# Kernel tuning notes

Hardware: AMD Instinct MI355X
Metric: run time of the kernel (lower is better)

Reference implementation:

```python
import jax, jax.numpy as jnp
import numpy as np

G = 16                 # grid side -> 4096 voxels
N_GRID = G ** 3
N_NODES = 4096         # protein nodes
DEG = 256              # node neighbors per grid voxel
HID = 64               # MPNN hidden == ResNet in_channels
NUM_CLASSES = 20
BN = np.float32(1.0 / np.sqrt(1.0 + 1e-5))  # eval-mode BatchNorm3d (mean=0, var=1, gamma=1, beta=0)


def _lin(key, fi, fo):
    return jax.random.normal(key, (fi, fo), jnp.float32) * (fi ** -0.5)


def _cw(key, o, i, k):
    return jax.random.normal(key, (o, i, k, k, k), jnp.float32) * ((i * k ** 3) ** -0.5)


def setup_inputs() -> dict:
    key = jax.random.key(0)
    ks = jax.random.split(key, 32)
    n_edges = N_GRID * DEG
    # every grid voxel receives exactly DEG messages (bincount never zero)
    edge_i = jax.random.randint(ks[0], (n_edges,), 0, N_NODES, dtype=jnp.int32)
    edge_j = jnp.repeat(jnp.arange(N_GRID, dtype=jnp.int32), DEG)
    edge_index = jnp.stack([edge_i, edge_j])  # [2, E]

    node_embedding = jax.random.normal(ks[1], (N_NODES, HID), jnp.float32)
    node_pos = jax.random.uniform(ks[2], (N_NODES, 3), jnp.float32)
    gx = (jnp.arange(G, dtype=jnp.float32) + 0.5) / G
    gd, gh, gw = jnp.meshgrid(gx, gx, gx, indexing='ij')
    grid_pos = jnp.stack([gd, gh, gw], -1).reshape(N_GRID, 3)

    z = lambda n: jnp.zeros((n,), jnp.float32)
    return {
        'node_embedding': node_embedding, 'node_pos': node_pos,
        'grid_pos': grid_pos, 'edge_index': edge_index,
        # MPNN edge / message / update MLPs
        'ew1': _lin(ks[3], 6, HID), 'eb1': z(HID), 'ew2': _lin(ks[4], HID, HID), 'eb2': z(HID),
        'mw1': _lin(ks[5], 2 * HID, HID), 'mb1': z(HID), 'mw2': _lin(ks[6], HID, HID), 'mb2': z(HID),
        'uw1': _lin(ks[7], HID, HID), 'ub1': z(HID), 'uw2': _lin(ks[8], HID, HID), 'ub2': z(HID),
        # ResNet3D: 3 Blocks (conv3 a, conv3 b, conv5 shortcut) with channels 64->64, 64->128, 128->256
        'c1a': _cw(ks[9], 64, 64, 3), 'c1b': _cw(ks[10], 64, 64, 3), 'c1s': _cw(ks[11], 64, 64, 5),
        'c2a': _cw(ks[12], 128, 64, 3), 'c2b': _cw(ks[13], 128, 128, 3), 'c2s': _cw(ks[14], 128, 64, 5),
        'c3a': _cw(ks[15], 256, 128, 3), 'c3b': _cw(ks[16], 256, 256, 3), 'c3s': _cw(ks[17], 256, 128, 5),
        'fcw': _lin(ks[18], 256, NUM_CLASSES), 'fcb': z(NUM_CLASSES),
    }


def _mlp(x, w1, b1, w2, b2):
    return jax.nn.silu(x @ w1 + b1) @ w2 + b2


def _conv(x, w, p):
    return jax.lax.conv_general_dilated(
        x, w, window_strides=(1, 1, 1), padding=[(p, p)] * 3,
        dimension_numbers=('NCDHW', 'OIDHW', 'NCDHW'))


def _block(x, wa, wb, ws):
    out = jax.nn.relu(_conv(x, wa, 1) * BN)
    out = _conv(out, wb, 1) * BN
    sc = _conv(x, ws, 2) * BN
    return jax.nn.relu(out + sc)


def reference(node_embedding, node_pos, grid_pos, edge_index,
              ew1, eb1, ew2, eb2, mw1, mb1, mw2, mb2, uw1, ub1, uw2, ub2,
              c1a, c1b, c1s, c2a, c2b, c2s, c3a, c3b, c3s, fcw, fcb):
    i, j = edge_index[0], edge_index[1]
    # ---- MPNN: gather, edge MLP, message MLP, scatter-mean, update MLP ----
    edge_attr = jnp.concatenate([node_pos[i], grid_pos[j]], axis=-1)        # [E, 6]
    pos_emb = _mlp(edge_attr, ew1, eb1, ew2, eb2)                           # [E, H]
    msg = _mlp(jnp.concatenate([node_embedding[i], pos_emb], -1),
               mw1, mb1, mw2, mb2)                                          # [E, H]
    agg = jax.ops.segment_sum(msg, j, num_segments=N_GRID)                  # [N_GRID, H]
    cnt = jax.ops.segment_sum(jnp.ones((msg.shape[0],), msg.dtype), j,
                              num_segments=N_GRID)
    grid_feat = _mlp(agg / cnt[:, None], uw1, ub1, uw2, ub2)                # [N_GRID, H]
    # ---- ResNet3D over the grid volume ----
    x = grid_feat.T.reshape(1, HID, G, G, G) * BN                           # instance_norm1 (eval BN)
    x = _block(x, c1a, c1b, c1s)
    x = _block(x, c2a, c2b, c2s)
    x = _block(x, c3a, c3b, c3s)
    pooled = jnp.max(x, axis=(2, 3, 4))                                     # max_pool3d(kernel=spatial)
    return pooled @ fcw + fcb                                               # [1, NUM_CLASSES]
```

## Files before the change

kernel.cpp:

```cpp
#include <hip/hip_runtime.h>
#include <math.h>

#define BN_S 0.9999950000374997f

typedef _Float16 half8 __attribute__((ext_vector_type(8)));
typedef float f32x4 __attribute__((ext_vector_type(4)));

__device__ __forceinline__ float silu_f(float x) {
    return __fdividef(x, 1.0f + __expf(-x));
}

__device__ __forceinline__ void gld16(const void* g, void* l) {
    __builtin_amdgcn_global_load_lds(
        (const __attribute__((address_space(1))) void*)g,
        (__attribute__((address_space(3))) void*)l, 16, 0, 0);
}

__global__ __launch_bounds__(64) void prep_w_k(
    const float* __restrict__ ew2, const float* __restrict__ mw1,
    const float* __restrict__ mw2, const float* __restrict__ uw1,
    const float* __restrict__ mb2, const float* __restrict__ ub1,
    float* __restrict__ W_mu, float* __restrict__ b_mu,
    _Float16* __restrict__ wemt_h, _Float16* __restrict__ wemt_l)
{
    const int k = blockIdx.x, c = threadIdx.x;
    float s = 0.f;
    for (int m = 0; m < 64; m++) s = fmaf(ew2[k*64 + m], mw1[(64 + m)*64 + c], s);
    {
        const int q = k >> 5, kg = (k >> 3) & 3, jj = k & 7;
        const int sl = q*256 + c*4 + kg;
        const int p = sl ^ ((sl >> 3) & 7);
        const _Float16 h = (_Float16)s;
        const _Float16 l = (_Float16)(s - (float)h);
        wemt_h[p*8 + jj] = h;
        wemt_l[p*8 + jj] = l;
    }
    float s2 = 0.f;
    for (int m = 0; m < 64; m++) s2 = fmaf(mw2[k*64 + m], uw1[m*64 + c], s2);
    W_mu[k*64 + c] = s2;
    if (k == 0) {
        float s3 = ub1[c];
        for (int m = 0; m < 64; m++) s3 = fmaf(mb2[m], uw1[m*64 + c], s3);
        b_mu[c] = s3;
    }
}

__global__ __launch_bounds__(64) void prep_nodes_k(
    const float* __restrict__ node_embedding, const float* __restrict__ node_pos,
    const float* __restrict__ grid_pos, const float* __restrict__ ew1,
    const float* __restrict__ eb1, const float* __restrict__ mw1,
    const float* __restrict__ mb1, const float* __restrict__ eb2,
    float* __restrict__ a_node, float* __restrict__ g_vox, float* __restrict__ n_node)
{
    const int v = blockIdx.x, c = threadIdx.x;
    const float p0 = node_pos[v*3], p1 = node_pos[v*3 + 1], p2 = node_pos[v*3 + 2];
    a_node[v*64 + c] = fmaf(p0, ew1[c], fmaf(p1, ew1[64 + c], fmaf(p2, ew1[128 + c], eb1[c])));
    const float q0 = grid_pos[v*3], q1 = grid_pos[v*3 + 1], q2 = grid_pos[v*3 + 2];
    g_vox[v*64 + c] = fmaf(q0, ew1[192 + c], fmaf(q1, ew1[256 + c], q2 * ew1[320 + c]));
    float s = mb1[c];
    for (int k = 0; k < 64; k++) s = fmaf(node_embedding[v*64 + k], mw1[k*64 + c], s);
    for (int k = 0; k < 64; k++) s = fmaf(eb2[k], mw1[(64 + k)*64 + c], s);
    n_node[v*64 + c] = s;
}

template<int K3, int NCOG, int NCH>
__global__ __launch_bounds__(256) void wsplit_k(
    const float* __restrict__ w, _Float16* __restrict__ dh, _Float16* __restrict__ dl,
    int CI)
{
    __shared__ float s[32*K3];
    const int co = blockIdx.x, cig = blockIdx.y, t = threadIdx.x;
    const float* src = w + ((size_t)co*CI + cig*32)*K3;
    for (int m = t; m < 32*K3; m += 256) s[m] = src[m];
    __syncthreads();
    const int coG = co >> 6, col = co & 63;
    for (int m = t; m < 32*K3; m += 256) {
        const int tap = m >> 5, cil = m & 31;
        const float x = s[cil*K3 + tap];
        const _Float16 h = (_Float16)x;
        const _Float16 l = (_Float16)(x - (float)h);
        const int b = cil >> 3, jj = cil & 7;
        const int sl = col*4 + b;
        const int p = sl ^ ((sl >> 3) & 7);
        const size_t base = ((size_t)(tap*NCOG + coG)*NCH + cig) * 2048;
        dh[base + p*8 + jj] = h;
        dl[base + p*8 + jj] = l;
    }
}

__global__ __launch_bounds__(256, 3) void edge_kernel(
    const int* __restrict__ edge_i,
    const float* __restrict__ a_node, const float* __restrict__ g_vox,
    const float* __restrict__ n_node,
    const _Float16* __restrict__ wemt_h, const _Float16* __restrict__ wemt_l,
    const float* __restrict__ W_mu, const float* __restrict__ b_mu,
    const float* __restrict__ uw2, const float* __restrict__ ub2,
    _Float16* __restrict__ x0h, _Float16* __restrict__ x0l)
{
    __shared__ __align__(16) _Float16 sAh[4096], sAl[4096];
    __shared__ __align__(16) _Float16 sBh[2][4096], sBl[2][4096];
    __shared__ float sV1[64], sV2[64], sRed[4*64];

    const int j = blockIdx.x, t = threadIdx.x;
    const int lane = t & 63, wv = t >> 6, ln15 = lane & 15, kg = lane >> 4;
    const int ebase = j << 8;

    gld16(wemt_h + t*8, &sAh[t*8]);
    gld16(wemt_h + 2048 + t*8, &sAh[2048 + t*8]);
    gld16(wemt_l + t*8, &sAl[t*8]);
    gld16(wemt_l + 2048 + t*8, &sAl[2048 + t*8]);

    const int r = t >> 2, sub = t & 3;
    float4 gv4[4];
    #pragma unroll
    for (int m4 = 0; m4 < 4; m4++)
        gv4[m4] = *(const float4*)&g_vox[j*64 + sub*16 + m4*4];

    float4 A[2][4], N[2][4];
    {
        const int iA = edge_i[ebase + r];
        #pragma unroll
        for (int m4 = 0; m4 < 4; m4++)
            A[0][m4] = *(const float4*)&a_node[(size_t)iA*64 + sub*16 + m4*4];
        #pragma unroll
        for (int eF = 0; eF < 4; eF++) {
            const int ieX = edge_i[ebase + eF*16 + ln15];
            N[0][eF] = *(const float4*)&n_node[(size_t)ieX*64 + wv*16 + kg*4];
        }
    }

    asm volatile("s_waitcnt vmcnt(0)" ::: "memory");
    __syncthreads();

    float psum[4] = {0.f, 0.f, 0.f, 0.f};

    #pragma unroll
    for (int T = 0; T < 4; T++) {
        const int par = T & 1;
        {
            float s1v[16];
            #pragma unroll
            for (int m4 = 0; m4 < 4; m4++) {
                const float4 a = A[par][m4], g = gv4[m4];
                s1v[m4*4 + 0] = silu_f(a.x + g.x);
                s1v[m4*4 + 1] = silu_f(a.y + g.y);
                s1v[m4*4 + 2] = silu_f(a.z + g.z);
                s1v[m4*4 + 3] = silu_f(a.w + g.w);
            }
            uint32_t hw[8], lw[8];
            #pragma unroll
            for (int m = 0; m < 8; m++) {
                const auto hp = __builtin_amdgcn_cvt_pkrtz(s1v[2*m], s1v[2*m + 1]);
                const float h0f = (float)hp[0], h1f = (float)hp[1];
                const auto lp = __builtin_amdgcn_cvt_pkrtz(s1v[2*m] - h0f, s1v[2*m + 1] - h1f);
                hw[m] = __builtin_bit_cast(uint32_t, hp);
                lw[m] = __builtin_bit_cast(uint32_t, lp);
            }
            const int q = sub >> 1, kg0 = (sub & 1) * 2;
            const int sl0 = (q*4 + kg0)*64 + r;
            const int sl1 = sl0 + 64;
            const int p0 = sl0 ^ ((sl0 >> 6) & 7);
            const int p1 = sl1 ^ ((sl1 >> 6) & 7);
            uint4 u;
            u.x = hw[0]; u.y = hw[1]; u.z = hw[2]; u.w = hw[3];
            *(uint4*)&sBh[par][p0*8] = u;
            u.x = hw[4]; u.y = hw[5]; u.z = hw[6]; u.w = hw[7];
            *(uint4*)&sBh[par][p1*8] = u;
            u.x = lw[0]; u.y = lw[1]; u.z = lw[2]; u.w = lw[3];
            *(uint4*)&sBl[par][p0*8] = u;
            u.x = lw[4]; u.y = lw[5]; u.z = lw[6]; u.w = lw[7];
            *(uint4*)&sBl[par][p1*8] = u;
        }
        if (T < 3) {
            const int b1 = ebase + (T + 1)*64;
            const int iA = edge_i[b1 + r];
            #pragma unroll
            for (int m4 = 0; m4 < 4; m4++)
                A[par ^ 1][m4] = *(const float4*)&a_node[(size_t)iA*64 + sub*16 + m4*4];
            #pragma unroll
            for (int eF = 0; eF < 4; eF++) {
                const int ieX = edge_i[b1 + eF*16 + ln15];
                N[par ^ 1][eF] = *(const float4*)&n_node[(size_t)ieX*64 + wv*16 + kg*4];
            }
        }
        __syncthreads();
        #pragma unroll
        for (int eF = 0; eF < 4; eF++) {
            const int e = eF*16 + ln15;
            f32x4 acc;
            {
                const float4 nv = N[par][eF];
                acc[0] = nv.x; acc[1] = nv.y; acc[2] = nv.z; acc[3] = nv.w;
            }
            #pragma unroll
            for (int q2 = 0; q2 < 2; q2++) {
                const int sa = q2*256 + (wv*16 + ln15)*4 + kg;
                const int pa = sa ^ ((sa >> 3) & 7);
                const half8 Ah = *(const half8*)&sAh[pa*8];
                const half8 Al = *(const half8*)&sAl[pa*8];
                const int sbs = (q2*4 + kg)*64 + e;
                const int pb = sbs ^ ((sbs >> 6) & 7);
                const half8 Bh = *(const half8*)&sBh[par][pb*8];
                const half8 Bl = *(const half8*)&sBl[par][pb*8];
                acc = __builtin_amdgcn_mfma_f32_16x16x32_f16(Ah, Bh, acc, 0, 0, 0);
                acc = __builtin_amdgcn_mfma_f32_16x16x32_f16(Ah, Bl, acc, 0, 0, 0);
                acc = __builtin_amdgcn_mfma_f32_16x16x32_f16(Al, Bh, acc, 0, 0, 0);
            }
            #pragma unroll
            for (int rg = 0; rg < 4; rg++) psum[rg] += silu_f(acc[rg]);
        }
    }

    #pragma unroll
    for (int rg = 0; rg < 4; rg++) {
        float v = psum[rg];
        v += __shfl_xor(v, 1, 64); v += __shfl_xor(v, 2, 64);
        v += __shfl_xor(v, 4, 64); v += __shfl_xor(v, 8, 64);
        psum[rg] = v;
    }
    __syncthreads();
    if (ln15 == 0) {
        #pragma unroll
        for (int rg = 0; rg < 4; rg++)
            sV1[wv*16 + kg*4 + rg] = psum[rg] * (1.0f / 256.0f);
    }
    __syncthreads();
    {
        const int c = t & 63, part = t >> 6;
        float h = (part == 0) ? b_mu[c] : 0.f;
        #pragma unroll
        for (int k2 = 0; k2 < 16; k2++) {
            const int k = part*16 + k2;
            h = fmaf(sV1[k], W_mu[k*64 + c], h);
        }
        sRed[part*64 + c] = h;
    }
    __syncthreads();
    if (t < 64)
        sV2[t] = silu_f(sRed[t] + sRed[64 + t] + sRed[128 + t] + sRed[192 + t]);
    __syncthreads();
    {
        const int c = t & 63, part = t >> 6;
        float g = (part == 0) ? ub2[c] : 0.f;
        #pragma unroll
        for (int k2 = 0; k2 < 16; k2++) {
            const int k = part*16 + k2;
            g = fmaf(sV2[k], uw2[k*64 + c], g);
        }
        sRed[part*64 + c] = g;
    }
    __syncthreads();
    if (t < 64) {
        const float val = (sRed[t] + sRed[64 + t] + sRed[128 + t] + sRed[192 + t]) * BN_S;
        const _Float16 hh = (_Float16)val;
        const _Float16 ll = (_Float16)(val - (float)hh);
        const int c = t, zz = j >> 8, v = j & 255;
        const int oct = (c >> 3) & 3;
        const int vsw = v ^ (oct << 1);
        const size_t a16 = ((size_t)((c >> 5)*16 + zz)*1024 + oct*256 + vsw)*8 + (c & 7);
        x0h[a16] = hh; x0l[a16] = ll;
    }
}

template<int KK, int CI, int NCO32, int CIS, bool SWZ>
__global__ __launch_bounds__(256, 4) void conv_mfma_k(
    const _Float16* __restrict__ xh, const _Float16* __restrict__ xl,
    const _Float16* __restrict__ wh, const _Float16* __restrict__ wl,
    float* __restrict__ slab)
{
    constexpr int P = KK/2, K2 = KK*KK, NCH = CI/32, NCHS = NCH/CIS;
    constexpr int CO = NCO32*32, NCOG64 = NCO32/2;

    int d0, coG32, zidx;
    if (SWZ) {
        const int lin = blockIdx.x + 16*(blockIdx.y + NCO32*blockIdx.z);
        const int xcd = lin & 7, rest = lin >> 3;
        const int i = rest & 15, gg = rest >> 4;
        const int g = gg*8 + xcd;
        d0 = i; coG32 = g % NCO32; zidx = g / NCO32;
    } else {
        d0 = blockIdx.x; coG32 = blockIdx.y; zidx = blockIdx.z;
    }
    const int co64G = coG32 >> 1, coHalf = coG32 & 1;
    const int cis = zidx / KK, kd = zidx % KK;
    const int t = threadIdx.x;
    const int lane = t & 63, wv = t >> 6;
    const int ln15 = lane & 15, kg = lane >> 4;

    float* sout = slab + ((size_t)zidx*CO + coG32*32)*4096 + d0*256;
    const int z = d0 + kd - P;
    if ((unsigned)z >= 16u) {
        for (int m = t; m < 32*256; m += 256)
            sout[(size_t)(m >> 8)*4096 + (m & 255)] = 0.f;
        return;
    }

    __shared__ __align__(16) _Float16 sXh[8192];
    __shared__ __align__(16) _Float16 sXl[8192];
    __shared__ __align__(16) _Float16 zb[8];
    if (t < 8) zb[t] = (_Float16)0.f;

    int aoff[2];
    #pragma unroll
    for (int cf = 0; cf < 2; cf++) {
        const int s = (coHalf*32 + cf*16 + ln15)*4 + kg;
        aoff[cf] = (s ^ ((s >> 3) & 7)) * 8;
    }

    auto stage_X = [&](int ch) {
        const size_t b16 = ((size_t)ch*16 + z) * 8192;
        #pragma unroll
        for (int q = 0; q < 4; q++) {
            gld16(xh + b16 + (q*256 + t)*8, &sXh[(q*256 + t)*8]);
            gld16(xl + b16 + (q*256 + t)*8, &sXl[(q*256 + t)*8]);
        }
    };
    auto loadA = [&](int ch, int t2, half8* Ah, half8* Al) {
        const size_t b = ((size_t)((kd*K2 + t2)*NCOG64 + co64G)*NCH + ch) * 2048;
        #pragma unroll
        for (int cf = 0; cf < 2; cf++) {
            Ah[cf] = *(const half8*)&wh[b + aoff[cf]];
            Al[cf] = *(const half8*)&wl[b + aoff[cf]];
        }
    };

    f32x4 acc[2][4];
    #pragma unroll
    for (int a = 0; a < 2; a++)
        #pragma unroll
        for (int b = 0; b < 4; b++)
            #pragma unroll
            for (int r2 = 0; r2 < 4; r2++) acc[a][b][r2] = 0.f;

    const int ch0 = cis * NCHS;
    half8 nAh[2], nAl[2];
    stage_X(ch0);
    loadA(ch0, 0, nAh, nAl);
    asm volatile("s_waitcnt vmcnt(0)" ::: "memory");
    __syncthreads();

    for (int cc = 0; cc < NCHS; cc++) {
        const int ch = ch0 + cc;
        for (int t2 = 0; t2 < K2; t2++) {
            half8 cAh[2], cAl[2];
            #pragma unroll
            for (int cf = 0; cf < 2; cf++) { cAh[cf] = nAh[cf]; cAl[cf] = nAl[cf]; }
            if (t2 + 1 < K2)          loadA(ch, t2 + 1, nAh, nAl);
            else if (cc + 1 < NCHS)   loadA(ch + 1, 0, nAh, nAl);

            const int kh = t2 / KK, kw = t2 % KK;
            __builtin_amdgcn_s_setprio(1);
            #pragma unroll
            for (int f = 0; f < 4; f++) {
                const int h_in = wv*4 + f + kh - P;
                if ((unsigned)h_in < 16u) {
                    const int w_in = ln15 + kw - P;
                    const bool ok = (unsigned)w_in < 16u;
                    const int slot = ok ? (kg*256 + h_in*16 + (w_in ^ (kg << 1))) : 0;
                    const half8 Bh = ok ? *(const half8*)&sXh[slot*8] : *(const half8*)zb;
                    const half8 Bl = ok ? *(const half8*)&sXl[slot*8] : *(const half8*)zb;
                    #pragma unroll
                    for (int cf = 0; cf < 2; cf++) {
                        acc[cf][f] = __builtin_amdgcn_mfma_f32_16x16x32_f16(cAh[cf], Bh, acc[cf][f], 0, 0, 0);
                        acc[cf][f] = __builtin_amdgcn_mfma_f32_16x16x32_f16(cAh[cf], Bl, acc[cf][f], 0, 0, 0);
                        acc[cf][f] = __builtin_amdgcn_mfma_f32_16x16x32_f16(cAl[cf], Bh, acc[cf][f], 0, 0, 0);
                    }
                }
            }
            __builtin_amdgcn_s_setprio(0);
        }
        if (cc + 1 < NCHS) {
            __syncthreads();
            stage_X(ch + 1);
            asm volatile("s_waitcnt vmcnt(0)" ::: "memory");
            __syncthreads();
        }
    }

    #pragma unroll
    for (int cf = 0; cf < 2; cf++)
        #pragma unroll
        for (int f = 0; f < 4; f++)
            #pragma unroll
            for (int r2 = 0; r2 < 4; r2++)
                sout[(size_t)(cf*16 + kg*4 + r2)*4096 + wv*64 + f*16 + ln15] = acc[cf][f][r2];
}

template<int S, int RMODE, int OUT>
__global__ __launch_bounds__(256) void reduce_k(
    const float* __restrict__ pbuf, const float* __restrict__ addsrc,
    float* __restrict__ outf, _Float16* __restrict__ oh, _Float16* __restrict__ ol,
    int CO)
{
    const int z = blockIdx.x, c8 = blockIdx.y, v = threadIdx.x;
    float val[8];
    #pragma unroll
    for (int jj = 0; jj < 8; jj++) {
        const int c = c8*8 + jj;
        float a = 0.f;
        #pragma unroll
        for (int s = 0; s < S; s++)
            a += pbuf[((size_t)s*CO + c)*4096 + z*256 + v];
        a *= BN_S;
        if (RMODE == 3) a += addsrc[(size_t)c*4096 + z*256 + v];
        if (RMODE != 2) a = fmaxf(a, 0.f);
        val[jj] = a;
    }
    if (OUT == 0) {
        #pragma unroll
        for (int jj = 0; jj < 8; jj++)
            outf[(size_t)(c8*8 + jj)*4096 + z*256 + v] = val[jj];
    } else if (OUT == 1) {
        half8 hv, lv;
        #pragma unroll
        for (int jj = 0; jj < 8; jj++) {
            hv[jj] = (_Float16)val[jj];
            lv[jj] = (_Float16)(val[jj] - (float)hv[jj]);
        }
        const int oct = c8 & 3;
        const int vsw = v ^ (oct << 1);
        const size_t a16 = ((size_t)((c8 >> 2)*16 + z)*1024 + oct*256 + vsw)*8;
        *(half8*)&oh[a16] = hv;
        *(half8*)&ol[a16] = lv;
    } else {
        __shared__ float sm[4][8];
        #pragma unroll
        for (int jj = 0; jj < 8; jj++) {
            float m = val[jj];
            m = fmaxf(m, __shfl_xor(m, 1, 64));  m = fmaxf(m, __shfl_xor(m, 2, 64));
            m = fmaxf(m, __shfl_xor(m, 4, 64));  m = fmaxf(m, __shfl_xor(m, 8, 64));
            m = fmaxf(m, __shfl_xor(m, 16, 64)); m = fmaxf(m, __shfl_xor(m, 32, 64));
            if ((v & 63) == 0) sm[v >> 6][jj] = m;
        }
        __syncthreads();
        if (v < 8) {
            const float m = fmaxf(fmaxf(sm[0][v], sm[1][v]), fmaxf(sm[2][v], sm[3][v]));
            outf[z*CO + c8*8 + v] = m;
        }
    }
}

__global__ __launch_bounds__(256) void fc_k(
    const float* __restrict__ pp, const float* __restrict__ fcw,
    const float* __restrict__ fcb, float* __restrict__ out)
{
    __shared__ float sp[256];
    const int t = threadIdx.x;
    float m = pp[t];
    for (int zz = 1; zz < 16; zz++) m = fmaxf(m, pp[zz*256 + t]);
    sp[t] = m;
    __syncthreads();
    if (t < 20) {
        float s = fcb[t];
        for (int c = 0; c < 256; c++) s = fmaf(sp[c], fcw[c*20 + t], s);
        out[t] = s;
    }
}

extern "C" void kernel_launch(void* const* d_in, const int* in_sizes, int n_in,
                              void* d_out, int out_size, void* d_ws, size_t ws_size,
                              hipStream_t stream)
{
    const float* node_embedding = (const float*)d_in[0];
    const float* node_pos       = (const float*)d_in[1];
    const float* grid_pos       = (const float*)d_in[2];
    const int*   edge_index     = (const int*)d_in[3];
    const float* ew1 = (const float*)d_in[4];
    const float* eb1 = (const float*)d_in[5];
    const float* ew2 = (const float*)d_in[6];
    const float* eb2 = (const float*)d_in[7];
    const float* mw1 = (const float*)d_in[8];
    const float* mb1 = (const float*)d_in[9];
    const float* mw2 = (const float*)d_in[10];
    const float* mb2 = (const float*)d_in[11];
    const float* uw1 = (const float*)d_in[12];
    const float* ub1 = (const float*)d_in[13];
    const float* uw2 = (const float*)d_in[14];
    const float* ub2 = (const float*)d_in[15];
    const float* c1a = (const float*)d_in[16];
    const float* c1b = (const float*)d_in[17];
    const float* c1s = (const float*)d_in[18];
    const float* c2a = (const float*)d_in[19];
    const float* c2b = (const float*)d_in[20];
    const float* c2s = (const float*)d_in[21];
    const float* c3a = (const float*)d_in[22];
    const float* c3b = (const float*)d_in[23];
    const float* c3s = (const float*)d_in[24];
    const float* fcw = (const float*)d_in[25];
    const float* fcb = (const float*)d_in[26];
    float* out = (float*)d_out;
    const int* edge_i = edge_index;

    float* ws = (float*)d_ws;
    float* a_node = ws;                ws += 262144;
    float* g_vox  = ws;                ws += 262144;
    float* n_node = ws;                ws += 262144;
    float* W_mu   = ws;                ws += 4096;
    float* b_mu   = ws;                ws += 64;
    _Float16* wemt_h = (_Float16*)ws;  ws += 2048;
    _Float16* wemt_l = (_Float16*)ws;  ws += 2048;
    _Float16* x0h = (_Float16*)ws;     ws += 131072;
    _Float16* x0l = (_Float16*)ws;     ws += 131072;
    _Float16* t2h = (_Float16*)ws;     ws += 262144;
    _Float16* t2l = (_Float16*)ws;     ws += 262144;
    _Float16* x2h = (_Float16*)ws;     ws += 262144;
    _Float16* x2l = (_Float16*)ws;     ws += 262144;
    _Float16* t3h = (_Float16*)ws;     ws += 524288;
    _Float16* t3l = (_Float16*)ws;     ws += 524288;
    float* u2 = ws;                    ws += 524288;
    float* u3 = ws;                    ws += 1048576;
    float* slab = ws;                  ws += 5242880;
    float* poolPart = ws;              ws += 4096;
    _Float16* wh = (_Float16*)ws;      ws += 4585472;
    _Float16* wl = (_Float16*)ws;      ws += 4585472;
    _Float16* t1h = (_Float16*)a_node;
    _Float16* t1l = (_Float16*)(a_node + 131072);
    float* u1 = g_vox;
    _Float16* x1h = (_Float16*)n_node;
    _Float16* x1l = (_Float16*)(n_node + 131072);

    _Float16* w1a_h = wh + 0;       _Float16* w1a_l = wl + 0;
    _Float16* w1b_h = wh + 110592;  _Float16* w1b_l = wl + 110592;
    _Float16* w1s_h = wh + 221184;  _Float16* w1s_l = wl + 221184;
    _Float16* w2a_h = wh + 733184;  _Float16* w2a_l = wl + 733184;
    _Float16* w2b_h = wh + 954368;  _Float16* w2b_l = wl + 954368;
    _Float16* w2s_h = wh + 1396736; _Float16* w2s_l = wl + 1396736;
    _Float16* w3a_h = wh + 2420736; _Float16* w3a_l = wl + 2420736;
    _Float16* w3b_h = wh + 3305472; _Float16* w3b_l = wl + 3305472;
    _Float16* w3s_h = wh + 5074944; _Float16* w3s_l = wl + 5074944;

    hipLaunchKernelGGL((wsplit_k<27,1,2>),  dim3(64,2),  dim3(256), 0, stream, c1a, w1a_h, w1a_l, 64);
    hipLaunchKernelGGL((wsplit_k<27,1,2>),  dim3(64,2),  dim3(256), 0, stream, c1b, w1b_h, w1b_l, 64);
    hipLaunchKernelGGL((wsplit_k<125,1,2>), dim3(64,2),  dim3(256), 0, stream, c1s, w1s_h, w1s_l, 64);
    hipLaunchKernelGGL((wsplit_k<27,2,2>),  dim3(128,2), dim3(256), 0, stream, c2a, w2a_h, w2a_l, 64);
    hipLaunchKernelGGL((wsplit_k<27,2,4>),  dim3(128,4), dim3(256), 0, stream, c2b, w2b_h, w2b_l, 128);
    hipLaunchKernelGGL((wsplit_k<125,2,2>), dim3(128,2), dim3(256), 0, stream, c2s, w2s_h, w2s_l, 64);
    hipLaunchKernelGGL((wsplit_k<27,4,4>),  dim3(256,4), dim3(256), 0, stream, c3a, w3a_h, w3a_l, 128);
    hipLaunchKernelGGL((wsplit_k<27,4,8>),  dim3(256,8), dim3(256), 0, stream, c3b, w3b_h, w3b_l, 256);
    hipLaunchKernelGGL((wsplit_k<125,4,4>), dim3(256,4), dim3(256), 0, stream, c3s, w3s_h, w3s_l, 128);

    hipLaunchKernelGGL(prep_w_k, dim3(64), dim3(64), 0, stream,
                       ew2, mw1, mw2, uw1, mb2, ub1, W_mu, b_mu, wemt_h, wemt_l);
    hipLaunchKernelGGL(prep_nodes_k, dim3(4096), dim3(64), 0, stream,
                       node_embedding, node_pos, grid_pos, ew1, eb1, mw1, mb1, eb2,
                       a_node, g_vox, n_node);
    hipLaunchKernelGGL(edge_kernel, dim3(4096), dim3(256), 0, stream,
                       edge_i, a_node, g_vox, n_node, wemt_h, wemt_l,
                       W_mu, b_mu, uw2, ub2, x0h, x0l);

    hipLaunchKernelGGL((conv_mfma_k<3,64,2,2,false>), dim3(16,2,6), dim3(256), 0, stream, x0h, x0l, w1a_h, w1a_l, slab);
    hipLaunchKernelGGL((reduce_k<6,1,1>), dim3(16,8), dim3(256), 0, stream, slab, (const float*)nullptr, (float*)nullptr, t1h, t1l, 64);
    hipLaunchKernelGGL((conv_mfma_k<3,64,2,2,false>), dim3(16,2,6), dim3(256), 0, stream, t1h, t1l, w1b_h, w1b_l, slab);
    hipLaunchKernelGGL((reduce_k<6,2,0>), dim3(16,8), dim3(256), 0, stream, slab, (const float*)nullptr, u1, (_Float16*)nullptr, (_Float16*)nullptr, 64);
    hipLaunchKernelGGL((conv_mfma_k<5,64,2,2,false>), dim3(16,2,10), dim3(256), 0, stream, x0h, x0l, w1s_h, w1s_l, slab);
    hipLaunchKernelGGL((reduce_k<10,3,1>), dim3(16,8), dim3(256), 0, stream, slab, u1, (float*)nullptr, x1h, x1l, 64);
    hipLaunchKernelGGL((conv_mfma_k<3,64,4,2,true>), dim3(16,4,6), dim3(256), 0, stream, x1h, x1l, w2a_h, w2a_l, slab);
    hipLaunchKernelGGL((reduce_k<6,1,1>), dim3(16,16), dim3(256), 0, stream, slab, (const float*)nullptr, (float*)nullptr, t2h, t2l, 128);
    hipLaunchKernelGGL((conv_mfma_k<3,128,4,2,true>), dim3(16,4,6), dim3(256), 0, stream, t2h, t2l, w2b_h, w2b_l, slab);
    hipLaunchKernelGGL((reduce_k<6,2,0>), dim3(16,16), dim3(256), 0, stream, slab, (const float*)nullptr, u2, (_Float16*)nullptr, (_Float16*)nullptr, 128);
    hipLaunchKernelGGL((conv_mfma_k<5,64,4,2,true>), dim3(16,4,10), dim3(256), 0, stream, x1h, x1l, w2s_h, w2s_l, slab);
    hipLaunchKernelGGL((reduce_k<10,3,1>), dim3(16,16), dim3(256), 0, stream, slab, u2, (float*)nullptr, x2h, x2l, 128);
    hipLaunchKernelGGL((conv_mfma_k<3,128,8,1,true>), dim3(16,8,3), dim3(256), 0, stream, x2h, x2l, w3a_h, w3a_l, slab);
    hipLaunchKernelGGL((reduce_k<3,1,1>), dim3(16,32), dim3(256), 0, stream, slab, (const float*)nullptr, (float*)nullptr, t3h, t3l, 256);
    hipLaunchKernelGGL((conv_mfma_k<3,256,8,1,true>), dim3(16,8,3), dim3(256), 0, stream, t3h, t3l, w3b_h, w3b_l, slab);
    hipLaunchKernelGGL((reduce_k<3,2,0>), dim3(16,32), dim3(256), 0, stream, slab, (const float*)nullptr, u3, (_Float16*)nullptr, (_Float16*)nullptr, 256);
    hipLaunchKernelGGL((conv_mfma_k<5,128,8,1,true>), dim3(16,8,5), dim3(256), 0, stream, x2h, x2l, w3s_h, w3s_l, slab);
    hipLaunchKernelGGL((reduce_k<5,3,2>), dim3(16,32), dim3(256), 0, stream, slab, u3, poolPart, (_Float16*)nullptr, (_Float16*)nullptr, 256);

    hipLaunchKernelGGL(fc_k, dim3(1), dim3(256), 0, stream, poolPart, fcw, fcb, out);

    (void)in_sizes; (void)n_in; (void)out_size; (void)ws_size;
}
```

Before: 538.2 us.

## Batch weight-split launches, merge prep kernels, halve channels per reduce block

```diff
diff --git a/kernel.cpp b/kernel.cpp
--- a/kernel.cpp
+++ b/kernel.cpp
@@ -16,43 +16,41 @@
         (__attribute__((address_space(3))) void*)l, 16, 0, 0);
 }
 
-__global__ __launch_bounds__(64) void prep_w_k(
-    const float* __restrict__ ew2, const float* __restrict__ mw1,
-    const float* __restrict__ mw2, const float* __restrict__ uw1,
-    const float* __restrict__ mb2, const float* __restrict__ ub1,
-    float* __restrict__ W_mu, float* __restrict__ b_mu,
-    _Float16* __restrict__ wemt_h, _Float16* __restrict__ wemt_l)
-{
-    const int k = blockIdx.x, c = threadIdx.x;
-    float s = 0.f;
-    for (int m = 0; m < 64; m++) s = fmaf(ew2[k*64 + m], mw1[(64 + m)*64 + c], s);
-    {
-        const int q = k >> 5, kg = (k >> 3) & 3, jj = k & 7;
-        const int sl = q*256 + c*4 + kg;
-        const int p = sl ^ ((sl >> 3) & 7);
-        const _Float16 h = (_Float16)s;
-        const _Float16 l = (_Float16)(s - (float)h);
-        wemt_h[p*8 + jj] = h;
-        wemt_l[p*8 + jj] = l;
-    }
-    float s2 = 0.f;
-    for (int m = 0; m < 64; m++) s2 = fmaf(mw2[k*64 + m], uw1[m*64 + c], s2);
-    W_mu[k*64 + c] = s2;
-    if (k == 0) {
-        float s3 = ub1[c];
-        for (int m = 0; m < 64; m++) s3 = fmaf(mb2[m], uw1[m*64 + c], s3);
-        b_mu[c] = s3;
-    }
-}
-
-__global__ __launch_bounds__(64) void prep_nodes_k(
+__global__ __launch_bounds__(64) void prep_all_k(
     const float* __restrict__ node_embedding, const float* __restrict__ node_pos,
     const float* __restrict__ grid_pos, const float* __restrict__ ew1,
     const float* __restrict__ eb1, const float* __restrict__ mw1,
     const float* __restrict__ mb1, const float* __restrict__ eb2,
-    float* __restrict__ a_node, float* __restrict__ g_vox, float* __restrict__ n_node)
+    const float* __restrict__ ew2, const float* __restrict__ mw2,
+    const float* __restrict__ uw1, const float* __restrict__ mb2,
+    const float* __restrict__ ub1,
+    float* __restrict__ a_node, float* __restrict__ g_vox, float* __restrict__ n_node,
+    float* __restrict__ W_mu, float* __restrict__ b_mu,
+    _Float16* __restrict__ wemt_h, _Float16* __restrict__ wemt_l)
 {
     const int v = blockIdx.x, c = threadIdx.x;
+    if (v < 64) {
+        const int k = v;
+        float s = 0.f;
+        for (int m = 0; m < 64; m++) s = fmaf(ew2[k*64 + m], mw1[(64 + m)*64 + c], s);
+        {
+            const int q = k >> 5, kg = (k >> 3) & 3, jj = k & 7;
+            const int sl = q*256 + c*4 + kg;
+            const int p = sl ^ ((sl >> 3) & 7);
+            const _Float16 h = (_Float16)s;
+            const _Float16 l = (_Float16)(s - (float)h);
+            wemt_h[p*8 + jj] = h;
+            wemt_l[p*8 + jj] = l;
+        }
+        float s2 = 0.f;
+        for (int m = 0; m < 64; m++) s2 = fmaf(mw2[k*64 + m], uw1[m*64 + c], s2);
+        W_mu[k*64 + c] = s2;
+        if (k == 0) {
+            float s3 = ub1[c];
+            for (int m = 0; m < 64; m++) s3 = fmaf(mb2[m], uw1[m*64 + c], s3);
+            b_mu[c] = s3;
+        }
+    }
     const float p0 = node_pos[v*3], p1 = node_pos[v*3 + 1], p2 = node_pos[v*3 + 2];
     a_node[v*64 + c] = fmaf(p0, ew1[c], fmaf(p1, ew1[64 + c], fmaf(p2, ew1[128 + c], eb1[c])));
     const float q0 = grid_pos[v*3], q1 = grid_pos[v*3 + 1], q2 = grid_pos[v*3 + 2];
@@ -63,17 +61,31 @@
     n_node[v*64 + c] = s;
 }
 
-template<int K3, int NCOG, int NCH>
-__global__ __launch_bounds__(256) void wsplit_k(
-    const float* __restrict__ w, _Float16* __restrict__ dh, _Float16* __restrict__ dl,
-    int CI)
+struct WSArgs {
+    const float* src[6];
+    _Float16* dh[6];
+    _Float16* dl[6];
+    int CI[6], NCOG[6], NCH[6];
+    int ofs[7];
+    int n;
+};
+
+template<int K3>
+__global__ __launch_bounds__(256) void wsplit_k(WSArgs a)
 {
     __shared__ float s[32*K3];
-    const int co = blockIdx.x, cig = blockIdx.y, t = threadIdx.x;
-    const float* src = w + ((size_t)co*CI + cig*32)*K3;
+    const int flat = blockIdx.x, t = threadIdx.x;
+    int i = 0;
+    while (i + 1 < a.n && flat >= a.ofs[i + 1]) i++;
+    const int local = flat - a.ofs[i];
+    const int NCH = a.NCH[i], NCOG = a.NCOG[i], CI = a.CI[i];
+    const int co = local / NCH, cig = local % NCH;
+    const float* src = a.src[i] + ((size_t)co*CI + cig*32)*K3;
     for (int m = t; m < 32*K3; m += 256) s[m] = src[m];
     __syncthreads();
     const int coG = co >> 6, col = co & 63;
+    _Float16* dh = a.dh[i];
+    _Float16* dl = a.dl[i];
     for (int m = t; m < 32*K3; m += 256) {
         const int tap = m >> 5, cil = m & 31;
         const float x = s[cil*K3 + tap];
@@ -392,11 +404,11 @@
     float* __restrict__ outf, _Float16* __restrict__ oh, _Float16* __restrict__ ol,
     int CO)
 {
-    const int z = blockIdx.x, c8 = blockIdx.y, v = threadIdx.x;
-    float val[8];
-    #pragma unroll
-    for (int jj = 0; jj < 8; jj++) {
-        const int c = c8*8 + jj;
+    const int z = blockIdx.x, c4 = blockIdx.y, v = threadIdx.x;
+    float val[4];
+    #pragma unroll
+    for (int jj = 0; jj < 4; jj++) {
+        const int c = c4*4 + jj;
         float a = 0.f;
         #pragma unroll
         for (int s = 0; s < S; s++)
@@ -408,24 +420,24 @@
     }
     if (OUT == 0) {
         #pragma unroll
-        for (int jj = 0; jj < 8; jj++)
-            outf[(size_t)(c8*8 + jj)*4096 + z*256 + v] = val[jj];
+        for (int jj = 0; jj < 4; jj++)
+            outf[(size_t)(c4*4 + jj)*4096 + z*256 + v] = val[jj];
     } else if (OUT == 1) {
-        half8 hv, lv;
-        #pragma unroll
-        for (int jj = 0; jj < 8; jj++) {
+        _Float16 hv[4], lv[4];
+        #pragma unroll
+        for (int jj = 0; jj < 4; jj++) {
             hv[jj] = (_Float16)val[jj];
             lv[jj] = (_Float16)(val[jj] - (float)hv[jj]);
         }
-        const int oct = c8 & 3;
+        const int oct = (c4 >> 1) & 3;
         const int vsw = v ^ (oct << 1);
-        const size_t a16 = ((size_t)((c8 >> 2)*16 + z)*1024 + oct*256 + vsw)*8;
-        *(half8*)&oh[a16] = hv;
-        *(half8*)&ol[a16] = lv;
+        const size_t a16 = (((size_t)(c4 >> 3)*16 + z)*1024 + oct*256 + vsw)*8 + (c4 & 1)*4;
+        *(uint2*)&oh[a16] = *(const uint2*)hv;
+        *(uint2*)&ol[a16] = *(const uint2*)lv;
     } else {
-        __shared__ float sm[4][8];
-        #pragma unroll
-        for (int jj = 0; jj < 8; jj++) {
+        __shared__ float sm[4][4];
+        #pragma unroll
+        for (int jj = 0; jj < 4; jj++) {
             float m = val[jj];
             m = fmaxf(m, __shfl_xor(m, 1, 64));  m = fmaxf(m, __shfl_xor(m, 2, 64));
             m = fmaxf(m, __shfl_xor(m, 4, 64));  m = fmaxf(m, __shfl_xor(m, 8, 64));
@@ -433,9 +445,9 @@
             if ((v & 63) == 0) sm[v >> 6][jj] = m;
         }
         __syncthreads();
-        if (v < 8) {
+        if (v < 4) {
             const float m = fmaxf(fmaxf(sm[0][v], sm[1][v]), fmaxf(sm[2][v], sm[3][v]));
-            outf[z*CO + c8*8 + v] = m;
+            outf[z*CO + c4*4 + v] = m;
         }
     }
 }
@@ -529,43 +541,55 @@
     _Float16* w3b_h = wh + 3305472; _Float16* w3b_l = wl + 3305472;
     _Float16* w3s_h = wh + 5074944; _Float16* w3s_l = wl + 5074944;
 
-    hipLaunchKernelGGL((wsplit_k<27,1,2>),  dim3(64,2),  dim3(256), 0, stream, c1a, w1a_h, w1a_l, 64);
-    hipLaunchKernelGGL((wsplit_k<27,1,2>),  dim3(64,2),  dim3(256), 0, stream, c1b, w1b_h, w1b_l, 64);
-    hipLaunchKernelGGL((wsplit_k<125,1,2>), dim3(64,2),  dim3(256), 0, stream, c1s, w1s_h, w1s_l, 64);
-    hipLaunchKernelGGL((wsplit_k<27,2,2>),  dim3(128,2), dim3(256), 0, stream, c2a, w2a_h, w2a_l, 64);
-    hipLaunchKernelGGL((wsplit_k<27,2,4>),  dim3(128,4), dim3(256), 0, stream, c2b, w2b_h, w2b_l, 128);
-    hipLaunchKernelGGL((wsplit_k<125,2,2>), dim3(128,2), dim3(256), 0, stream, c2s, w2s_h, w2s_l, 64);
-    hipLaunchKernelGGL((wsplit_k<27,4,4>),  dim3(256,4), dim3(256), 0, stream, c3a, w3a_h, w3a_l, 128);
-    hipLaunchKernelGGL((wsplit_k<27,4,8>),  dim3(256,8), dim3(256), 0, stream, c3b, w3b_h, w3b_l, 256);
-    hipLaunchKernelGGL((wsplit_k<125,4,4>), dim3(256,4), dim3(256), 0, stream, c3s, w3s_h, w3s_l, 128);
-
-    hipLaunchKernelGGL(prep_w_k, dim3(64), dim3(64), 0, stream,
-                       ew2, mw1, mw2, uw1, mb2, ub1, W_mu, b_mu, wemt_h, wemt_l);
-    hipLaunchKernelGGL(prep_nodes_k, dim3(4096), dim3(64), 0, stream,
+    {
+        WSArgs a27;
+        a27.n = 6;
+        a27.src[0] = c1a; a27.dh[0] = w1a_h; a27.dl[0] = w1a_l; a27.CI[0] = 64;  a27.NCOG[0] = 1; a27.NCH[0] = 2;
+        a27.src[1] = c1b; a27.dh[1] = w1b_h; a27.dl[1] = w1b_l; a27.CI[1] = 64;  a27.NCOG[1] = 1; a27.NCH[1] = 2;
+        a27.src[2] = c2a; a27.dh[2] = w2a_h; a27.dl[2] = w2a_l; a27.CI[2] = 64;  a27.NCOG[2] = 2; a27.NCH[2] = 2;
+        a27.src[3] = c2b; a27.dh[3] = w2b_h; a27.dl[3] = w2b_l; a27.CI[3] = 128; a27.NCOG[3] = 2; a27.NCH[3] = 4;
+        a27.src[4] = c3a; a27.dh[4] = w3a_h; a27.dl[4] = w3a_l; a27.CI[4] = 128; a27.NCOG[4] = 4; a27.NCH[4] = 4;
+        a27.src[5] = c3b; a27.dh[5] = w3b_h; a27.dl[5] = w3b_l; a27.CI[5] = 256; a27.NCOG[5] = 4; a27.NCH[5] = 8;
+        a27.ofs[0] = 0;    a27.ofs[1] = 128;  a27.ofs[2] = 256;  a27.ofs[3] = 512;
+        a27.ofs[4] = 1024; a27.ofs[5] = 2048; a27.ofs[6] = 4096;
+        hipLaunchKernelGGL((wsplit_k<27>), dim3(4096), dim3(256), 0, stream, a27);
+
+        WSArgs a125;
+        a125.n = 3;
+        a125.src[0] = c1s; a125.dh[0] = w1s_h; a125.dl[0] = w1s_l; a125.CI[0] = 64;  a125.NCOG[0] = 1; a125.NCH[0] = 2;
+        a125.src[1] = c2s; a125.dh[1] = w2s_h; a125.dl[1] = w2s_l; a125.CI[1] = 64;  a125.NCOG[1] = 2; a125.NCH[1] = 2;
+        a125.src[2] = c3s; a125.dh[2] = w3s_h; a125.dl[2] = w3s_l; a125.CI[2] = 128; a125.NCOG[2] = 4; a125.NCH[2] = 4;
+        a125.ofs[0] = 0; a125.ofs[1] = 128; a125.ofs[2] = 384; a125.ofs[3] = 1408;
+        a125.ofs[4] = 0; a125.ofs[5] = 0; a125.ofs[6] = 0;
+        hipLaunchKernelGGL((wsplit_k<125>), dim3(1408), dim3(256), 0, stream, a125);
+    }
+
+    hipLaunchKernelGGL(prep_all_k, dim3(4096), dim3(64), 0, stream,
                        node_embedding, node_pos, grid_pos, ew1, eb1, mw1, mb1, eb2,
-                       a_node, g_vox, n_node);
+                       ew2, mw2, uw1, mb2, ub1,
+                       a_node, g_vox, n_node, W_mu, b_mu, wemt_h, wemt_l);
     hipLaunchKernelGGL(edge_kernel, dim3(4096), dim3(256), 0, stream,
                        edge_i, a_node, g_vox, n_node, wemt_h, wemt_l,
                        W_mu, b_mu, uw2, ub2, x0h, x0l);
 
     hipLaunchKernelGGL((conv_mfma_k<3,64,2,2,false>), dim3(16,2,6), dim3(256), 0, stream, x0h, x0l, w1a_h, w1a_l, slab);
-    hipLaunchKernelGGL((reduce_k<6,1,1>), dim3(16,8), dim3(256), 0, stream, slab, (const float*)nullptr, (float*)nullptr, t1h, t1l, 64);
+    hipLaunchKernelGGL((reduce_k<6,1,1>), dim3(16,16), dim3(256), 0, stream, slab, (const float*)nullptr, (float*)nullptr, t1h, t1l, 64);
     hipLaunchKernelGGL((conv_mfma_k<3,64,2,2,false>), dim3(16,2,6), dim3(256), 0, stream, t1h, t1l, w1b_h, w1b_l, slab);
-    hipLaunchKernelGGL((reduce_k<6,2,0>), dim3(16,8), dim3(256), 0, stream, slab, (const float*)nullptr, u1, (_Float16*)nullptr, (_Float16*)nullptr, 64);
+    hipLaunchKernelGGL((reduce_k<6,2,0>), dim3(16,16), dim3(256), 0, stream, slab, (const float*)nullptr, u1, (_Float16*)nullptr, (_Float16*)nullptr, 64);
     hipLaunchKernelGGL((conv_mfma_k<5,64,2,2,false>), dim3(16,2,10), dim3(256), 0, stream, x0h, x0l, w1s_h, w1s_l, slab);
-    hipLaunchKernelGGL((reduce_k<10,3,1>), dim3(16,8), dim3(256), 0, stream, slab, u1, (float*)nullptr, x1h, x1l, 64);
+    hipLaunchKernelGGL((reduce_k<10,3,1>), dim3(16,16), dim3(256), 0, stream, slab, u1, (float*)nullptr, x1h, x1l, 64);
     hipLaunchKernelGGL((conv_mfma_k<3,64,4,2,true>), dim3(16,4,6), dim3(256), 0, stream, x1h, x1l, w2a_h, w2a_l, slab);
-    hipLaunchKernelGGL((reduce_k<6,1,1>), dim3(16,16), dim3(256), 0, stream, slab, (const float*)nullptr, (float*)nullptr, t2h, t2l, 128);
+    hipLaunchKernelGGL((reduce_k<6,1,1>), dim3(16,32), dim3(256), 0, stream, slab, (const float*)nullptr, (float*)nullptr, t2h, t2l, 128);
     hipLaunchKernelGGL((conv_mfma_k<3,128,4,2,true>), dim3(16,4,6), dim3(256), 0, stream, t2h, t2l, w2b_h, w2b_l, slab);
-    hipLaunchKernelGGL((reduce_k<6,2,0>), dim3(16,16), dim3(256), 0, stream, slab, (const float*)nullptr, u2, (_Float16*)nullptr, (_Float16*)nullptr, 128);
+    hipLaunchKernelGGL((reduce_k<6,2,0>), dim3(16,32), dim3(256), 0, stream, slab, (const float*)nullptr, u2, (_Float16*)nullptr, (_Float16*)nullptr, 128);
     hipLaunchKernelGGL((conv_mfma_k<5,64,4,2,true>), dim3(16,4,10), dim3(256), 0, stream, x1h, x1l, w2s_h, w2s_l, slab);
-    hipLaunchKernelGGL((reduce_k<10,3,1>), dim3(16,16), dim3(256), 0, stream, slab, u2, (float*)nullptr, x2h, x2l, 128);
+    hipLaunchKernelGGL((reduce_k<10,3,1>), dim3(16,32), dim3(256), 0, stream, slab, u2, (float*)nullptr, x2h, x2l, 128);
     hipLaunchKernelGGL((conv_mfma_k<3,128,8,1,true>), dim3(16,8,3), dim3(256), 0, stream, x2h, x2l, w3a_h, w3a_l, slab);
-    hipLaunchKernelGGL((reduce_k<3,1,1>), dim3(16,32), dim3(256), 0, stream, slab, (const float*)nullptr, (float*)nullptr, t3h, t3l, 256);
+    hipLaunchKernelGGL((reduce_k<3,1,1>), dim3(16,64), dim3(256), 0, stream, slab, (const float*)nullptr, (float*)nullptr, t3h, t3l, 256);
     hipLaunchKernelGGL((conv_mfma_k<3,256,8,1,true>), dim3(16,8,3), dim3(256), 0, stream, t3h, t3l, w3b_h, w3b_l, slab);
-    hipLaunchKernelGGL((reduce_k<3,2,0>), dim3(16,32), dim3(256), 0, stream, slab, (const float*)nullptr, u3, (_Float16*)nullptr, (_Float16*)nullptr, 256);
+    hipLaunchKernelGGL((reduce_k<3,2,0>), dim3(16,64), dim3(256), 0, stream, slab, (const float*)nullptr, u3, (_Float16*)nullptr, (_Float16*)nullptr, 256);
     hipLaunchKernelGGL((conv_mfma_k<5,128,8,1,true>), dim3(16,8,5), dim3(256), 0, stream, x2h, x2l, w3s_h, w3s_l, slab);
-    hipLaunchKernelGGL((reduce_k<5,3,2>), dim3(16,32), dim3(256), 0, stream, slab, u3, poolPart, (_Float16*)nullptr, (_Float16*)nullptr, 256);
+    hipLaunchKernelGGL((reduce_k<5,3,2>), dim3(16,64), dim3(256), 0, stream, slab, u3, poolPart, (_Float16*)nullptr, (_Float16*)nullptr, 256);
 
     hipLaunchKernelGGL(fc_k, dim3(1), dim3(256), 0, stream, poolPart, fcw, fcb, out);
 
```

Result: faster. 479.0 us (median of 2 runs) (-11.0%).
